# Performance work log

Measured on AMD Instinct MI355X. Metric: run time of the kernel, lower is better.

Reference implementation:

```python
import jax, jax.numpy as jnp
import numpy as np

NUM_HEADS = 8
B, S, D = 4, 2048, 512


def setup_inputs() -> dict:
    key = jax.random.key(0)
    ks = jax.random.split(key, 12)
    scale = 1.0 / np.sqrt(D)
    return {
        "v": jax.random.normal(ks[0], (B, S, D), dtype=jnp.float32),
        "k": jax.random.normal(ks[1], (B, S, D), dtype=jnp.float32),
        "q": jax.random.normal(ks[2], (B, S, D), dtype=jnp.float32),
        "Wq": jax.random.normal(ks[3], (D, D), dtype=jnp.float32) * scale,
        "bq": jnp.zeros((D,), dtype=jnp.float32),
        "Wk": jax.random.normal(ks[4], (D, D), dtype=jnp.float32) * scale,
        "bk": jnp.zeros((D,), dtype=jnp.float32),
        "Wv": jax.random.normal(ks[5], (D, D), dtype=jnp.float32) * scale,
        "bv": jnp.zeros((D,), dtype=jnp.float32),
        "Wo": jax.random.normal(ks[6], (D, D), dtype=jnp.float32) * scale,
        "bo": jnp.zeros((D,), dtype=jnp.float32),
        "top_k": 32,
    }


def reference(v, k, q, Wq, bq, Wk, bk, Wv, bv, Wo, bo, top_k):
    dh = D // NUM_HEADS  # per-head depth

    def split_heads(x):  # [B,S,D] -> [B,H,S,dh]
        return x.reshape(B, -1, NUM_HEADS, dh).transpose(0, 2, 1, 3)

    qh = split_heads(q @ Wq + bq)
    kh = split_heads(k @ Wk + bk)
    vh = split_heads(v @ Wv + bv)

    logits = jnp.einsum('bhqd,bhkd->bhqk', qh, kh) / jnp.sqrt(jnp.float32(dh))
    w = jax.nn.softmax(logits, axis=-1)  # [B,H,S,S]

    num_keys = w.shape[-1]
    if top_k < num_keys:
        vals, idx = jax.lax.top_k(w, top_k)  # [B,H,S,top_k]
        bb = jnp.arange(B)[:, None, None, None]
        hh = jnp.arange(NUM_HEADS)[None, :, None, None]
        qq = jnp.arange(S)[None, None, :, None]
        sparse = jnp.zeros_like(w).at[bb, hh, qq, idx].set(vals)
        # tf.linalg.normalize(ord=1): divide by L1 norm along last axis
        w = sparse / jnp.sum(jnp.abs(sparse), axis=-1, keepdims=True)

    attn = jnp.einsum('bhqk,bhkd->bhqd', w, vh)  # [B,H,S,dh]
    concat = attn.transpose(0, 2, 1, 3).reshape(B, -1, D)
    out = concat @ Wo + bo
    return (out, w)
```

## Files before the change

kernel.cpp:

```cpp
#include <hip/hip_runtime.h>
#include <hip/hip_bf16.h>
#include <stdint.h>

#define S_LEN 2048
#define DMODEL 512
#define NH 8
#define DH 64
#define TOPK 32
#define CMAX 128
#define LO_SCALE 4096.0f
#define INV_LO (1.0f/4096.0f)

typedef _Float16 f16;
typedef f16 half8 __attribute__((ext_vector_type(8)));
typedef f16 half4 __attribute__((ext_vector_type(4)));
typedef float floatx4 __attribute__((ext_vector_type(4)));
typedef float f32x4 __attribute__((ext_vector_type(4)));

#define AS1 __attribute__((address_space(1)))
#define AS3 __attribute__((address_space(3)))

__device__ __forceinline__ void gl_lds16(const void* g, void* l) {
    __builtin_amdgcn_global_load_lds((const AS1 void*)g, (AS3 void*)l, 16, 0, 0);
}
__device__ __forceinline__ void lds_fence() {
    asm volatile("s_waitcnt lgkmcnt(0)" ::: "memory");
}

__global__ __launch_bounds__(256, 2)
void qkproj(const float* __restrict__ Xq, const float* __restrict__ Xk,
            const float* __restrict__ Wq_, const float* __restrict__ Wk_,
            const float* __restrict__ bq_, const float* __restrict__ bk_,
            float* __restrict__ outQ, float* __restrict__ outK)
{
    __shared__ float As[32][132];
    __shared__ float Bs[32][264];
    const float* X    = blockIdx.z ? Xk  : Xq;
    const float* W    = blockIdx.z ? Wk_ : Wq_;
    const float* bias = blockIdx.z ? bk_ : bq_;
    float* out        = blockIdx.z ? outK : outQ;
    const int tid = threadIdx.x;
    const int tx = tid & 15;
    const int ty = tid >> 4;
    const int m0 = blockIdx.y * 128;
    const int n0 = blockIdx.x * 256;

    float acc[8][16];
#pragma unroll
    for (int i = 0; i < 8; ++i)
#pragma unroll
        for (int j = 0; j < 16; ++j) acc[i][j] = 0.f;

    f32x4 pa[4];
#pragma unroll
    for (int u = 0; u < 4; ++u) {
        int id = tid + u * 256;
        pa[u] = *(const f32x4*)(X + (size_t)(m0 + (id >> 3)) * 512 + (id & 7) * 4);
    }

    for (int k0 = 0; k0 < 512; k0 += 32) {
#pragma unroll
        for (int u = 0; u < 4; ++u) {
            int id = tid + u * 256;
            int r = id >> 3, c4 = (id & 7) * 4;
            As[c4 + 0][r] = pa[u].x; As[c4 + 1][r] = pa[u].y;
            As[c4 + 2][r] = pa[u].z; As[c4 + 3][r] = pa[u].w;
        }
#pragma unroll
        for (int u = 0; u < 8; ++u) {
            int id = tid + u * 256;
            int rb = id >> 6, cb = (id & 63) * 4;
            *(f32x4*)&Bs[rb][cb] = *(const f32x4*)(W + (size_t)(k0 + rb) * 512 + n0 + cb);
        }
        __syncthreads();
        if (k0 < 480) {
            int kn = k0 + 32;
#pragma unroll
            for (int u = 0; u < 4; ++u) {
                int id = tid + u * 256;
                pa[u] = *(const f32x4*)(X + (size_t)(m0 + (id >> 3)) * 512 + kn + (id & 7) * 4);
            }
        }
#pragma unroll 8
        for (int kk = 0; kk < 32; ++kk) {
            float a[8], b[16];
            *(f32x4*)&a[0] = *(const f32x4*)&As[kk][ty * 4];
            *(f32x4*)&a[4] = *(const f32x4*)&As[kk][64 + ty * 4];
#pragma unroll
            for (int h = 0; h < 4; ++h)
                *(f32x4*)&b[h * 4] = *(const f32x4*)&Bs[kk][tx * 4 + h * 64];
#pragma unroll
            for (int i = 0; i < 8; ++i)
#pragma unroll
                for (int j = 0; j < 16; ++j)
                    acc[i][j] = fmaf(a[i], b[j], acc[i][j]);
        }
        __syncthreads();
    }

    float bb[16];
#pragma unroll
    for (int h = 0; h < 4; ++h)
        *(f32x4*)&bb[h * 4] = *(const f32x4*)(bias + n0 + h * 64 + tx * 4);

#pragma unroll
    for (int i = 0; i < 8; ++i) {
        int r = m0 + (i >> 2) * 64 + ty * 4 + (i & 3);
        int b_ = r >> 11, s = r & 2047;
#pragma unroll
        for (int h = 0; h < 4; ++h) {
            int c = n0 + h * 64 + tx * 4;
            f32x4 w = {acc[i][h * 4 + 0] + bb[h * 4 + 0],
                       acc[i][h * 4 + 1] + bb[h * 4 + 1],
                       acc[i][h * 4 + 2] + bb[h * 4 + 2],
                       acc[i][h * 4 + 3] + bb[h * 4 + 3]};
            int hd = c >> 6, d = c & 63;
            float* p = out + (((size_t)(b_ * NH + hd) * S_LEN) + s) * DH + d;
            *(f32x4*)p = w;
        }
    }
}

__global__ __launch_bounds__(256, 2)
void gemm_logits(const float* __restrict__ Qh, const float* __restrict__ Kh,
                 float* __restrict__ logits)
{
    __shared__ float As[32][132];
    __shared__ float Bs[32][260];
    const int tid = threadIdx.x;
    const int tx = tid & 15;
    const int ty = tid >> 4;
    const int bh = blockIdx.z;
    const float* Ab = Qh + (size_t)bh * S_LEN * DH;
    const float* Bb = Kh + (size_t)bh * S_LEN * DH;
    const int q0 = blockIdx.y * 128;
    const int k0 = blockIdx.x * 256;

    float acc[8][16];
#pragma unroll
    for (int i = 0; i < 8; ++i)
#pragma unroll
        for (int j = 0; j < 16; ++j) acc[i][j] = 0.f;

    f32x4 qa[4], kb[8];
#pragma unroll
    for (int u = 0; u < 4; ++u) {
        int id = tid + u * 256;
        qa[u] = *(const f32x4*)(Ab + (size_t)(q0 + (id >> 3)) * DH + (id & 7) * 4);
    }
#pragma unroll
    for (int u = 0; u < 8; ++u) {
        int id = tid + u * 256;
        kb[u] = *(const f32x4*)(Bb + (size_t)(k0 + (id >> 3)) * DH + (id & 7) * 4);
    }

    for (int ch = 0; ch < 2; ++ch) {
#pragma unroll
        for (int u = 0; u < 4; ++u) {
            int id = tid + u * 256;
            int r = id >> 3, c4 = (id & 7) * 4;
            As[c4 + 0][r] = qa[u].x * 0.125f; As[c4 + 1][r] = qa[u].y * 0.125f;
            As[c4 + 2][r] = qa[u].z * 0.125f; As[c4 + 3][r] = qa[u].w * 0.125f;
        }
#pragma unroll
        for (int u = 0; u < 8; ++u) {
            int id = tid + u * 256;
            int r = id >> 3, c4 = (id & 7) * 4;
            Bs[c4 + 0][r] = kb[u].x; Bs[c4 + 1][r] = kb[u].y;
            Bs[c4 + 2][r] = kb[u].z; Bs[c4 + 3][r] = kb[u].w;
        }
        __syncthreads();
        if (ch == 0) {
#pragma unroll
            for (int u = 0; u < 4; ++u) {
                int id = tid + u * 256;
                qa[u] = *(const f32x4*)(Ab + (size_t)(q0 + (id >> 3)) * DH + 32 + (id & 7) * 4);
            }
#pragma unroll
            for (int u = 0; u < 8; ++u) {
                int id = tid + u * 256;
                kb[u] = *(const f32x4*)(Bb + (size_t)(k0 + (id >> 3)) * DH + 32 + (id & 7) * 4);
            }
        }
#pragma unroll 8
        for (int kk = 0; kk < 32; ++kk) {
            float a[8], b[16];
            *(f32x4*)&a[0] = *(const f32x4*)&As[kk][ty * 4];
            *(f32x4*)&a[4] = *(const f32x4*)&As[kk][64 + ty * 4];
#pragma unroll
            for (int h = 0; h < 4; ++h)
                *(f32x4*)&b[h * 4] = *(const f32x4*)&Bs[kk][tx * 4 + h * 64];
#pragma unroll
            for (int i = 0; i < 8; ++i)
#pragma unroll
                for (int j = 0; j < 16; ++j)
                    acc[i][j] = fmaf(a[i], b[j], acc[i][j]);
        }
        __syncthreads();
    }

#pragma unroll
    for (int i = 0; i < 8; ++i) {
        int r = q0 + (i >> 2) * 64 + ty * 4 + (i & 3);
        float* C = logits + (size_t)bh * S_LEN * S_LEN + (size_t)r * S_LEN + k0;
#pragma unroll
        for (int h = 0; h < 4; ++h) {
            f32x4 v = {acc[i][h * 4 + 0], acc[i][h * 4 + 1],
                       acc[i][h * 4 + 2], acc[i][h * 4 + 3]};
            __builtin_nontemporal_store(v, (f32x4*)(C + h * 64 + tx * 4));
        }
    }
}

__global__ __launch_bounds__(256)
void wsplit2(const float* __restrict__ W0, const float* __restrict__ W1,
             f16* __restrict__ planes)
{
    __shared__ float tile[32][33];
    const float* W = blockIdx.z ? W1 : W0;
    f16* Th = planes + (size_t)blockIdx.z * 524288;
    f16* Tl = Th + 262144;
    const int bx = blockIdx.x * 32;
    const int by = blockIdx.y * 32;
    const int lx = threadIdx.x & 31, ly = threadIdx.x >> 5;
#pragma unroll
    for (int r = ly; r < 32; r += 8)
        tile[r][lx] = W[(size_t)(by + r) * 512 + bx + lx];
    __syncthreads();
#pragma unroll
    for (int r = ly; r < 32; r += 8) {
        float x = tile[lx][r];
        f16 h = (f16)x;
        f16 l = (f16)((x - (float)h) * LO_SCALE);
        Th[(size_t)(bx + r) * 512 + by + lx] = h;
        Tl[(size_t)(bx + r) * 512 + by + lx] = l;
    }
}

__global__ __launch_bounds__(256)
void gemm_x32(const float* __restrict__ X,
              const f16* __restrict__ Bh_, const f16* __restrict__ Bl_,
              const float* __restrict__ bias, float* __restrict__ outF, int mode)
{
    __shared__ f16 sm[16384];
    f16* As_h = sm;       f16* As_l = sm + 4096;
    f16* Bs_h = sm + 8192; f16* Bs_l = sm + 12288;
    const int tid  = threadIdx.x;
    const int lane = tid & 63, wv = tid >> 6;
    const int wm = wv & 1, wn = wv >> 1;
    const int quad = lane >> 4, l15 = lane & 15;
    const int m0 = blockIdx.y * 128, n0 = blockIdx.x * 128;

    floatx4 acc_h[4][4], acc_c[4][4];
    const floatx4 z4 = {0.f, 0.f, 0.f, 0.f};
#pragma unroll
    for (int i = 0; i < 4; ++i)
#pragma unroll
        for (int j = 0; j < 4; ++j) { acc_h[i][j] = z4; acc_c[i][j] = z4; }

    for (int k0 = 0; k0 < 512; k0 += 32) {
        __syncthreads();
#pragma unroll
        for (int c = 0; c < 4; ++c) {
            int r   = c * 32 + (tid >> 3);
            int col = (tid & 7) * 4;
            f32x4 x = *(const f32x4*)(X + (size_t)(m0 + r) * 512 + k0 + col);
            f16 h0 = (f16)x.x, h1 = (f16)x.y, h2 = (f16)x.z, h3 = (f16)x.w;
            half4 hv = {h0, h1, h2, h3};
            half4 lv = {(f16)((x.x - (float)h0) * LO_SCALE),
                        (f16)((x.y - (float)h1) * LO_SCALE),
                        (f16)((x.z - (float)h2) * LO_SCALE),
                        (f16)((x.w - (float)h3) * LO_SCALE)};
            *(half4*)&As_h[r * 32 + col] = hv;
            *(half4*)&As_l[r * 32 + col] = lv;
        }
#pragma unroll
        for (int c = 0; c < 2; ++c) {
            int r    = c * 64 + (wv << 4) + (lane >> 2);
            int ch   = (lane & 3) * 8;
            int lidx = (c * 64 + (wv << 4)) * 32 + lane * 8;
            gl_lds16(Bh_ + (size_t)(n0 + r) * 512 + k0 + ch, &Bs_h[lidx]);
            gl_lds16(Bl_ + (size_t)(n0 + r) * 512 + k0 + ch, &Bs_l[lidx]);
        }
        asm volatile("s_waitcnt vmcnt(0)" ::: "memory");
        __syncthreads();

        half8 bh8[4], bl8[4];
#pragma unroll
        for (int j = 0; j < 4; ++j) {
            int n = wn * 64 + j * 16 + l15;
            bh8[j] = *(const half8*)&Bs_h[n * 32 + quad * 8];
            bl8[j] = *(const half8*)&Bs_l[n * 32 + quad * 8];
        }
#pragma unroll
        for (int i = 0; i < 4; ++i) {
            int m = wm * 64 + i * 16 + l15;
            half8 ah = *(const half8*)&As_h[m * 32 + quad * 8];
            half8 al = *(const half8*)&As_l[m * 32 + quad * 8];
#pragma unroll
            for (int j = 0; j < 4; ++j) {
                acc_h[i][j] = __builtin_amdgcn_mfma_f32_16x16x32_f16(ah, bh8[j], acc_h[i][j], 0, 0, 0);
                acc_c[i][j] = __builtin_amdgcn_mfma_f32_16x16x32_f16(ah, bl8[j], acc_c[i][j], 0, 0, 0);
                acc_c[i][j] = __builtin_amdgcn_mfma_f32_16x16x32_f16(al, bh8[j], acc_c[i][j], 0, 0, 0);
            }
        }
    }

#pragma unroll
    for (int j = 0; j < 4; ++j) {
        int col = n0 + wn * 64 + j * 16 + l15;
        float bv = bias[col];
#pragma unroll
        for (int i = 0; i < 4; ++i) {
            int rbase = m0 + wm * 64 + i * 16 + quad * 4;
#pragma unroll
            for (int rg = 0; rg < 4; ++rg) {
                float r = acc_h[i][j][rg] + acc_c[i][j][rg] * INV_LO + bv;
                int row = rbase + rg;
                if (mode == 2) {
                    outF[(size_t)row * 512 + col] = r;
                } else {
                    int b_ = row >> 11, s = row & 2047, h = col >> 6, d = col & 63;
                    outF[(((size_t)(b_ * NH + h)) * S_LEN + s) * DH + d] = r;
                }
            }
        }
    }
}

__global__ __launch_bounds__(256)
void gemm_x16(const f16* __restrict__ Ah_, const f16* __restrict__ Al_,
              const f16* __restrict__ Bh_, const f16* __restrict__ Bl_,
              const float* __restrict__ bias, float* __restrict__ outF,
              int Ksz, int ldc, int mode)
{
    __shared__ f16 sm[16384];
    f16* As_h = sm;        f16* As_l = sm + 4096;
    f16* Bs_h = sm + 8192; f16* Bs_l = sm + 12288;
    const int tid  = threadIdx.x;
    const int lane = tid & 63, wv = tid >> 6;
    const int wm = wv & 1, wn = wv >> 1;
    const int quad = lane >> 4, l15 = lane & 15;
    const int m0 = blockIdx.y * 128, n0 = blockIdx.x * 128;

    floatx4 acc_h[4][4], acc_c[4][4];
    const floatx4 z4 = {0.f, 0.f, 0.f, 0.f};
#pragma unroll
    for (int i = 0; i < 4; ++i)
#pragma unroll
        for (int j = 0; j < 4; ++j) { acc_h[i][j] = z4; acc_c[i][j] = z4; }

    for (int k0 = 0; k0 < Ksz; k0 += 32) {
        __syncthreads();
#pragma unroll
        for (int c = 0; c < 2; ++c) {
            int r    = c * 64 + (wv << 4) + (lane >> 2);
            int ch   = (lane & 3) * 8;
            int lidx = (c * 64 + (wv << 4)) * 32 + lane * 8;
            gl_lds16(Ah_ + (size_t)(m0 + r) * Ksz + k0 + ch, &As_h[lidx]);
            gl_lds16(Al_ + (size_t)(m0 + r) * Ksz + k0 + ch, &As_l[lidx]);
            gl_lds16(Bh_ + (size_t)(n0 + r) * Ksz + k0 + ch, &Bs_h[lidx]);
            gl_lds16(Bl_ + (size_t)(n0 + r) * Ksz + k0 + ch, &Bs_l[lidx]);
        }
        asm volatile("s_waitcnt vmcnt(0)" ::: "memory");
        __syncthreads();

        half8 bh8[4], bl8[4];
#pragma unroll
        for (int j = 0; j < 4; ++j) {
            int n = wn * 64 + j * 16 + l15;
            bh8[j] = *(const half8*)&Bs_h[n * 32 + quad * 8];
            bl8[j] = *(const half8*)&Bs_l[n * 32 + quad * 8];
        }
#pragma unroll
        for (int i = 0; i < 4; ++i) {
            int m = wm * 64 + i * 16 + l15;
            half8 ah = *(const half8*)&As_h[m * 32 + quad * 8];
            half8 al = *(const half8*)&As_l[m * 32 + quad * 8];
#pragma unroll
            for (int j = 0; j < 4; ++j) {
                acc_h[i][j] = __builtin_amdgcn_mfma_f32_16x16x32_f16(ah, bh8[j], acc_h[i][j], 0, 0, 0);
                acc_c[i][j] = __builtin_amdgcn_mfma_f32_16x16x32_f16(ah, bl8[j], acc_c[i][j], 0, 0, 0);
                acc_c[i][j] = __builtin_amdgcn_mfma_f32_16x16x32_f16(al, bh8[j], acc_c[i][j], 0, 0, 0);
            }
        }
    }

#pragma unroll
    for (int j = 0; j < 4; ++j) {
        int col = n0 + wn * 64 + j * 16 + l15;
        float bv = (mode == 2) ? bias[col] : 0.f;
#pragma unroll
        for (int i = 0; i < 4; ++i) {
            int rbase = m0 + wm * 64 + i * 16 + quad * 4;
#pragma unroll
            for (int rg = 0; rg < 4; ++rg) {
                float r = acc_h[i][j][rg] + acc_c[i][j][rg] * INV_LO;
                int row = rbase + rg;
                outF[(size_t)row * ldc + col] = r + bv;
            }
        }
    }
}

__device__ __forceinline__ unsigned sortable_u(float f) {
    unsigned u = __float_as_uint(f);
    return u ^ ((unsigned)(((int)u) >> 31) | 0x80000000u);
}

__global__ __launch_bounds__(256)
void topk_attn(float* __restrict__ wbuf, const float* __restrict__ Vh,
               f16* __restrict__ attH, f16* __restrict__ attL)
{
    __shared__ float    wrow[4][2048];
    __shared__ uint64_t cand[4][CMAX];
    __shared__ float    win_w[4][TOPK];
    __shared__ int      win_i[4][TOPK];

    const int tid  = threadIdx.x;
    const int wv   = tid >> 6;
    const int lane = tid & 63;
    const unsigned long long lt = (1ull << lane) - 1ull;
    const int row = blockIdx.x * 4 + wv;
    float* wr = wbuf + (size_t)row * 2048;

    if (lane < TOPK) { win_w[wv][lane] = 0.f; win_i[wv][lane] = 0; }

    float L[32];
#pragma unroll
    for (int t = 0; t < 8; ++t) {
        f32x4 x = __builtin_nontemporal_load((const f32x4*)(wr + t * 256 + lane * 4));
        L[4 * t + 0] = x.x; L[4 * t + 1] = x.y; L[4 * t + 2] = x.z; L[4 * t + 3] = x.w;
    }

    const f32x4 z = {0.f, 0.f, 0.f, 0.f};
#pragma unroll
    for (int t = 0; t < 8; ++t) ((f32x4*)wrow[wv])[t * 64 + lane] = z;

    float m = L[0];
#pragma unroll
    for (int t = 1; t < 32; ++t) m = fmaxf(m, L[t]);
#pragma unroll
    for (int off = 32; off > 0; off >>= 1) m = fmaxf(m, __shfl_xor(m, off, 64));

    auto wcount = [&](float T) -> int {
        int c = 0;
#pragma unroll
        for (int t = 0; t < 32; ++t) c += (int)__popcll(__ballot(L[t] >= T));
        return c;
    };

    float delta = 2.f;
    int clo = wcount(m - delta);
    int guard = 0;
    while (clo < TOPK && guard < 8) { delta *= 16.f; clo = wcount(m - delta); ++guard; }
    float Tlo = m - delta, Thi = m;
    guard = 0;
    while (clo > 64 && guard < 40) {
        float mid = 0.5f * (Tlo + Thi);
        int cc = wcount(mid);
        if (cc >= TOPK) { Tlo = mid; clo = cc; } else { Thi = mid; }
        ++guard;
    }
    const int nc = min(clo, CMAX);

    int base = 0;
#pragma unroll
    for (int t = 0; t < 32; ++t) {
        bool p = (L[t] >= Tlo);
        unsigned long long mk = __ballot(p);
        if (p) {
            int pos = base + (int)__popcll(mk & lt);
            if (pos < CMAX) {
                int idx = (t >> 2) * 256 + (lane << 2) + (t & 3);
                cand[wv][pos] = ((uint64_t)sortable_u(L[t]) << 32) | (uint32_t)(~(uint32_t)idx);
            }
        }
        base += (int)__popcll(mk);
    }
    lds_fence();

    float mysum = 0.f;
    int wbase = 0;
    const int passes = (nc + 63) >> 6;
    for (int it = 0; it < passes; ++it) {
        int ci = (it << 6) + lane;
        bool have = ci < nc;
        uint64_t mykey = have ? cand[wv][ci] : 0ull;
        int rank = 0;
#pragma unroll 8
        for (int j = 0; j < nc; ++j)
            rank += (cand[wv][j] > mykey) ? 1 : 0;
        bool win = have && (rank < TOPK);
        unsigned long long mk = __ballot(win);
        if (win) {
            int pos = wbase + (int)__popcll(mk & lt);
            unsigned uv = (unsigned)(mykey >> 32);
            unsigned fu = (uv & 0x80000000u) ? (uv ^ 0x80000000u) : ~uv;
            float v = __uint_as_float(fu);
            int idx = (int)(~(uint32_t)mykey);
            float e = __expf(v - m);
            win_w[wv][pos] = e;
            win_i[wv][pos] = idx;
            mysum += e;
        }
        wbase += (int)__popcll(mk);
    }
#pragma unroll
    for (int off = 32; off > 0; off >>= 1) mysum += __shfl_xor(mysum, off, 64);
    const float rw = 1.f / mysum;
    lds_fence();

    if (lane < TOPK) wrow[wv][win_i[wv][lane] & 2047] = win_w[wv][lane] * rw;
    lds_fence();

#pragma unroll
    for (int t = 0; t < 8; ++t)
        __builtin_nontemporal_store(((f32x4*)wrow[wv])[t * 64 + lane],
                                    (f32x4*)(wr + (size_t)(t * 64 + lane) * 4));

    const int bh = row >> 11;
    const float* Vb = Vh + (size_t)bh * S_LEN * DH;
    float acc = 0.f;
#pragma unroll
    for (int j = 0; j < TOPK; ++j) {
        float wj = win_w[wv][j] * rw;
        int   kj = win_i[wv][j];
        acc = fmaf(wj, Vb[(size_t)kj * DH + lane], acc);
    }
    const int b_ = row >> 14;
    const int h  = (row >> 11) & 7;
    const int s  = row & 2047;
    size_t oidx = (((size_t)b_ * S_LEN) + s) * 512 + h * DH + lane;
    f16 hh = (f16)acc;
    attH[oidx] = hh;
    attL[oidx] = (f16)((acc - (float)hh) * LO_SCALE);
}

extern "C" void kernel_launch(void* const* d_in, const int* in_sizes, int n_in,
                              void* d_out, int out_size, void* d_ws, size_t ws_size,
                              hipStream_t stream) {
    const float* v  = (const float*)d_in[0];
    const float* k  = (const float*)d_in[1];
    const float* q  = (const float*)d_in[2];
    const float* Wq = (const float*)d_in[3];
    const float* bq = (const float*)d_in[4];
    const float* Wk = (const float*)d_in[5];
    const float* bk = (const float*)d_in[6];
    const float* Wv = (const float*)d_in[7];
    const float* bv = (const float*)d_in[8];
    const float* Wo = (const float*)d_in[9];
    const float* bo = (const float*)d_in[10];

    float* out  = (float*)d_out;
    float* wout = out + (size_t)4 * S_LEN * 512;

    char* ws = (char*)d_ws;
    float* Vh   = (float*)ws;
    float* Qh32 = (float*)(ws + 16777216);
    float* Kh32 = (float*)(ws + 33554432);
    f16* WT  = (f16*)(ws + 50331648);
    f16 *WvH = WT,           *WvL = WT + 262144;
    f16 *WoH = WT + 524288,  *WoL = WT + 786432;
    f16* attH = (f16*)(ws + 16777216);
    f16* attL = (f16*)(ws + 25165824);

    wsplit2<<<dim3(16, 16, 2), 256, 0, stream>>>(Wv, Wo, WT);

    qkproj<<<dim3(2, 64, 2), 256, 0, stream>>>(q, k, Wq, Wk, bq, bk, Qh32, Kh32);
    gemm_x32<<<dim3(4, 64), 256, 0, stream>>>(v, WvH, WvL, bv, Vh, 1);

    gemm_logits<<<dim3(8, 16, 32), 256, 0, stream>>>(Qh32, Kh32, wout);

    topk_attn<<<16384, 256, 0, stream>>>(wout, Vh, attH, attL);

    gemm_x16<<<dim3(4, 64, 1), 256, 0, stream>>>(attH, attL, WoH, WoL, bo, out, 512, 512, 2);
}
```

Baseline: 1.120 ms.

## Fuse top-k selection into logits GEMM and shrink qkproj tile

The logits kernel now loops over all 2048 keys per 128-query block and keeps a running per-row top-32 list using a register bitonic sort plus a ballot-based insertion. This avoids writing and re-reading the full 2048x2048 logits matrix per head. Only the 32 packed key/index pairs are written to the start of each row, and a slimmer scatter kernel turns them into softmax weights and the dense output row. qkproj also drops to a 128-wide N tile with register-prefetched W loads. In exchange the grid is much smaller (512 blocks) and the serial insertion loop can diverge, so occupancy and latency hiding may suffer.

```diff
diff --git a/kernel.cpp b/kernel.cpp
--- a/kernel.cpp
+++ b/kernel.cpp
@@ -7,7 +7,6 @@
 #define NH 8
 #define DH 64
 #define TOPK 32
-#define CMAX 128
 #define LO_SCALE 4096.0f
 #define INV_LO (1.0f/4096.0f)
 
@@ -16,6 +15,7 @@
 typedef f16 half4 __attribute__((ext_vector_type(4)));
 typedef float floatx4 __attribute__((ext_vector_type(4)));
 typedef float f32x4 __attribute__((ext_vector_type(4)));
+typedef unsigned long long u64k;
 
 #define AS1 __attribute__((address_space(1)))
 #define AS3 __attribute__((address_space(3)))
@@ -27,14 +27,20 @@
     asm volatile("s_waitcnt lgkmcnt(0)" ::: "memory");
 }
 
-__global__ __launch_bounds__(256, 2)
+__device__ __forceinline__ u64k make_key(float f, int idx) {
+    unsigned u = __float_as_uint(f);
+    unsigned sv = u ^ ((unsigned)(((int)u) >> 31) | 0x80000000u);
+    return ((u64k)sv << 16) | (u64k)(0xFFFFu - (unsigned)idx);
+}
+
+__global__ __launch_bounds__(256)
 void qkproj(const float* __restrict__ Xq, const float* __restrict__ Xk,
             const float* __restrict__ Wq_, const float* __restrict__ Wk_,
             const float* __restrict__ bq_, const float* __restrict__ bk_,
             float* __restrict__ outQ, float* __restrict__ outK)
 {
     __shared__ float As[32][132];
-    __shared__ float Bs[32][264];
+    __shared__ float Bs[32][132];
     const float* X    = blockIdx.z ? Xk  : Xq;
     const float* W    = blockIdx.z ? Wk_ : Wq_;
     const float* bias = blockIdx.z ? bk_ : bq_;
@@ -43,19 +49,20 @@
     const int tx = tid & 15;
     const int ty = tid >> 4;
     const int m0 = blockIdx.y * 128;
-    const int n0 = blockIdx.x * 256;
-
-    float acc[8][16];
+    const int n0 = blockIdx.x * 128;
+
+    float acc[8][8];
 #pragma unroll
     for (int i = 0; i < 8; ++i)
 #pragma unroll
-        for (int j = 0; j < 16; ++j) acc[i][j] = 0.f;
-
-    f32x4 pa[4];
+        for (int j = 0; j < 8; ++j) acc[i][j] = 0.f;
+
+    f32x4 pa[4], pb[4];
 #pragma unroll
     for (int u = 0; u < 4; ++u) {
         int id = tid + u * 256;
         pa[u] = *(const f32x4*)(X + (size_t)(m0 + (id >> 3)) * 512 + (id & 7) * 4);
+        pb[u] = *(const f32x4*)(W + (size_t)(id >> 5) * 512 + n0 + (id & 31) * 4);
     }
 
     for (int k0 = 0; k0 < 512; k0 += 32) {
@@ -65,12 +72,8 @@
             int r = id >> 3, c4 = (id & 7) * 4;
             As[c4 + 0][r] = pa[u].x; As[c4 + 1][r] = pa[u].y;
             As[c4 + 2][r] = pa[u].z; As[c4 + 3][r] = pa[u].w;
-        }
-#pragma unroll
-        for (int u = 0; u < 8; ++u) {
-            int id = tid + u * 256;
-            int rb = id >> 6, cb = (id & 63) * 4;
-            *(f32x4*)&Bs[rb][cb] = *(const f32x4*)(W + (size_t)(k0 + rb) * 512 + n0 + cb);
+            int rb = id >> 5, cb = (id & 31) * 4;
+            *(f32x4*)&Bs[rb][cb] = pb[u];
         }
         __syncthreads();
         if (k0 < 480) {
@@ -79,36 +82,35 @@
             for (int u = 0; u < 4; ++u) {
                 int id = tid + u * 256;
                 pa[u] = *(const f32x4*)(X + (size_t)(m0 + (id >> 3)) * 512 + kn + (id & 7) * 4);
+                pb[u] = *(const f32x4*)(W + (size_t)(kn + (id >> 5)) * 512 + n0 + (id & 31) * 4);
             }
         }
 #pragma unroll 8
         for (int kk = 0; kk < 32; ++kk) {
-            float a[8], b[16];
+            float a[8], b[8];
             *(f32x4*)&a[0] = *(const f32x4*)&As[kk][ty * 4];
             *(f32x4*)&a[4] = *(const f32x4*)&As[kk][64 + ty * 4];
-#pragma unroll
-            for (int h = 0; h < 4; ++h)
-                *(f32x4*)&b[h * 4] = *(const f32x4*)&Bs[kk][tx * 4 + h * 64];
+            *(f32x4*)&b[0] = *(const f32x4*)&Bs[kk][tx * 4];
+            *(f32x4*)&b[4] = *(const f32x4*)&Bs[kk][64 + tx * 4];
 #pragma unroll
             for (int i = 0; i < 8; ++i)
 #pragma unroll
-                for (int j = 0; j < 16; ++j)
+                for (int j = 0; j < 8; ++j)
                     acc[i][j] = fmaf(a[i], b[j], acc[i][j]);
         }
         __syncthreads();
     }
 
-    float bb[16];
-#pragma unroll
-    for (int h = 0; h < 4; ++h)
-        *(f32x4*)&bb[h * 4] = *(const f32x4*)(bias + n0 + h * 64 + tx * 4);
+    float bb[8];
+    *(f32x4*)&bb[0] = *(const f32x4*)(bias + n0 + tx * 4);
+    *(f32x4*)&bb[4] = *(const f32x4*)(bias + n0 + 64 + tx * 4);
 
 #pragma unroll
     for (int i = 0; i < 8; ++i) {
-        int r = m0 + (i >> 2) * 64 + ty * 4 + (i & 3);
+        int r = m0 + ((i >> 2) << 6) + ty * 4 + (i & 3);
         int b_ = r >> 11, s = r & 2047;
 #pragma unroll
-        for (int h = 0; h < 4; ++h) {
+        for (int h = 0; h < 2; ++h) {
             int c = n0 + h * 64 + tx * 4;
             f32x4 w = {acc[i][h * 4 + 0] + bb[h * 4 + 0],
                        acc[i][h * 4 + 1] + bb[h * 4 + 1],
@@ -122,19 +124,19 @@
 }
 
 __global__ __launch_bounds__(256, 2)
-void gemm_logits(const float* __restrict__ Qh, const float* __restrict__ Kh,
-                 float* __restrict__ logits)
+void logits_topk(const float* __restrict__ Qh, const float* __restrict__ Kh,
+                 float* __restrict__ wbuf)
 {
-    __shared__ float As[32][132];
+    __shared__ float As[2][32][132];
     __shared__ float Bs[32][260];
     const int tid = threadIdx.x;
-    const int tx = tid & 15;
-    const int ty = tid >> 4;
-    const int bh = blockIdx.z;
+    const int lig = tid & 15;
+    const int ty  = tid >> 4;
+    const int gsh = ((tid & 63) >> 4) << 4;
+    const int bh = blockIdx.y;
+    const int q0 = blockIdx.x * 128;
     const float* Ab = Qh + (size_t)bh * S_LEN * DH;
     const float* Bb = Kh + (size_t)bh * S_LEN * DH;
-    const int q0 = blockIdx.y * 128;
-    const int k0 = blockIdx.x * 256;
 
     float acc[8][16];
 #pragma unroll
@@ -142,73 +144,144 @@
 #pragma unroll
         for (int j = 0; j < 16; ++j) acc[i][j] = 0.f;
 
-    f32x4 qa[4], kb[8];
-#pragma unroll
-    for (int u = 0; u < 4; ++u) {
-        int id = tid + u * 256;
-        qa[u] = *(const f32x4*)(Ab + (size_t)(q0 + (id >> 3)) * DH + (id & 7) * 4);
-    }
-#pragma unroll
-    for (int u = 0; u < 8; ++u) {
-        int id = tid + u * 256;
-        kb[u] = *(const f32x4*)(Bb + (size_t)(k0 + (id >> 3)) * DH + (id & 7) * 4);
-    }
-
-    for (int ch = 0; ch < 2; ++ch) {
-#pragma unroll
-        for (int u = 0; u < 4; ++u) {
-            int id = tid + u * 256;
-            int r = id >> 3, c4 = (id & 7) * 4;
-            As[c4 + 0][r] = qa[u].x * 0.125f; As[c4 + 1][r] = qa[u].y * 0.125f;
-            As[c4 + 2][r] = qa[u].z * 0.125f; As[c4 + 3][r] = qa[u].w * 0.125f;
-        }
+    u64k key0[8], key1[8];
+#pragma unroll
+    for (int i = 0; i < 8; ++i) { key0[i] = 0; key1[i] = 0; }
+
+    {
+        const int c4 = lig * 4;
+        const int ch = c4 >> 5;
+        const int cl = c4 & 31;
 #pragma unroll
         for (int u = 0; u < 8; ++u) {
-            int id = tid + u * 256;
-            int r = id >> 3, c4 = (id & 7) * 4;
-            Bs[c4 + 0][r] = kb[u].x; Bs[c4 + 1][r] = kb[u].y;
-            Bs[c4 + 2][r] = kb[u].z; Bs[c4 + 3][r] = kb[u].w;
-        }
-        __syncthreads();
-        if (ch == 0) {
-#pragma unroll
-            for (int u = 0; u < 4; ++u) {
-                int id = tid + u * 256;
-                qa[u] = *(const f32x4*)(Ab + (size_t)(q0 + (id >> 3)) * DH + 32 + (id & 7) * 4);
-            }
+            int r = ty + u * 16;
+            f32x4 x = *(const f32x4*)(Ab + (size_t)(q0 + r) * DH + c4);
+            As[ch][cl + 0][r] = x.x * 0.125f;
+            As[ch][cl + 1][r] = x.y * 0.125f;
+            As[ch][cl + 2][r] = x.z * 0.125f;
+            As[ch][cl + 3][r] = x.w * 0.125f;
+        }
+    }
+
+#pragma unroll 1
+    for (int kp = 0; kp < 8; ++kp) {
+#pragma unroll
+        for (int ch = 0; ch < 2; ++ch) {
+            f32x4 kb[8];
 #pragma unroll
             for (int u = 0; u < 8; ++u) {
                 int id = tid + u * 256;
-                kb[u] = *(const f32x4*)(Bb + (size_t)(k0 + (id >> 3)) * DH + 32 + (id & 7) * 4);
-            }
-        }
+                int r = id >> 3, c4 = (id & 7) * 4;
+                kb[u] = *(const f32x4*)(Bb + (size_t)(kp * 256 + r) * DH + ch * 32 + c4);
+            }
+            __syncthreads();
+#pragma unroll
+            for (int u = 0; u < 8; ++u) {
+                int id = tid + u * 256;
+                int r = id >> 3, c4 = (id & 7) * 4;
+                Bs[c4 + 0][r] = kb[u].x; Bs[c4 + 1][r] = kb[u].y;
+                Bs[c4 + 2][r] = kb[u].z; Bs[c4 + 3][r] = kb[u].w;
+            }
+            __syncthreads();
 #pragma unroll 8
-        for (int kk = 0; kk < 32; ++kk) {
-            float a[8], b[16];
-            *(f32x4*)&a[0] = *(const f32x4*)&As[kk][ty * 4];
-            *(f32x4*)&a[4] = *(const f32x4*)&As[kk][64 + ty * 4];
-#pragma unroll
-            for (int h = 0; h < 4; ++h)
-                *(f32x4*)&b[h * 4] = *(const f32x4*)&Bs[kk][tx * 4 + h * 64];
-#pragma unroll
-            for (int i = 0; i < 8; ++i)
-#pragma unroll
-                for (int j = 0; j < 16; ++j)
-                    acc[i][j] = fmaf(a[i], b[j], acc[i][j]);
-        }
-        __syncthreads();
+            for (int kk = 0; kk < 32; ++kk) {
+                float a[8], b[16];
+                *(f32x4*)&a[0] = *(const f32x4*)&As[ch][kk][ty * 4];
+                *(f32x4*)&a[4] = *(const f32x4*)&As[ch][kk][64 + ty * 4];
+#pragma unroll
+                for (int h = 0; h < 4; ++h)
+                    *(f32x4*)&b[h * 4] = *(const f32x4*)&Bs[kk][lig * 4 + h * 64];
+#pragma unroll
+                for (int i = 0; i < 8; ++i)
+#pragma unroll
+                    for (int j = 0; j < 16; ++j)
+                        acc[i][j] = fmaf(a[i], b[j], acc[i][j]);
+            }
+        }
+
+#pragma unroll
+        for (int i = 0; i < 8; ++i) {
+            int j0 = -1, j1 = -1;
+            if (kp == 0) {
+                u64k t0 = 0, t1 = 0;
+#pragma unroll
+                for (int j = 0; j < 16; ++j) {
+                    u64k kj = make_key(acc[i][j], ((j >> 2) << 6) + (lig << 2) + (j & 3));
+                    if (kj > t0)      { t1 = t0; j1 = j0; t0 = kj; j0 = j; }
+                    else if (kj > t1) { t1 = kj; j1 = j; }
+                }
+                key0[i] = t0; key1[i] = t1;
+#pragma unroll
+                for (int s = 2; s <= 32; s <<= 1) {
+#pragma unroll
+                    for (int d = s >> 1; d >= 1; d >>= 1) {
+                        int e0 = 2 * lig;
+                        if (d == 1) {
+                            bool descB = ((e0 & s) == 0);
+                            u64k mx = key0[i] > key1[i] ? key0[i] : key1[i];
+                            u64k mn = key0[i] > key1[i] ? key1[i] : key0[i];
+                            key0[i] = descB ? mx : mn;
+                            key1[i] = descB ? mn : mx;
+                        } else {
+                            bool descB = ((e0 & s) == 0);
+                            bool amS   = ((e0 & d) == 0);
+                            bool wantMax = (descB == amS);
+                            u64k p0 = __shfl_xor(key0[i], d >> 1, 16);
+                            u64k p1 = __shfl_xor(key1[i], d >> 1, 16);
+                            key0[i] = wantMax ? (key0[i] > p0 ? key0[i] : p0)
+                                              : (key0[i] > p0 ? p0 : key0[i]);
+                            key1[i] = wantMax ? (key1[i] > p1 ? key1[i] : p1)
+                                              : (key1[i] > p1 ? p1 : key1[i]);
+                        }
+                    }
+                }
+            }
+            u64k bot0 = __shfl(key1[i], 15, 16);
+            unsigned pend = 0;
+#pragma unroll
+            for (int j = 0; j < 16; ++j) {
+                u64k kj = make_key(acc[i][j], kp * 256 + ((j >> 2) << 6) + (lig << 2) + (j & 3));
+                if (kj > bot0 && j != j0 && j != j1) pend |= (1u << j);
+            }
+            for (int it = 0; it < 300; ++it) {
+                unsigned long long wb = __ballot(pend != 0);
+                unsigned gm = (unsigned)((wb >> gsh) & 0xFFFFull);
+                if (!gm) break;
+                int src = __ffs((int)gm) - 1;
+                int myj = __ffs((int)pend) - 1;
+                float mv = acc[i][0];
+#pragma unroll
+                for (int j = 1; j < 16; ++j) if (myj == j) mv = acc[i][j];
+                int jj = myj < 0 ? 0 : myj;
+                u64k ck = make_key(mv, kp * 256 + ((jj >> 2) << 6) + (lig << 2) + (jj & 3));
+                ck = __shfl(ck, src, 16);
+                if (lig == src) pend &= pend - 1;
+                u64k bt = __shfl(key1[i], 15, 16);
+                if (ck <= bt) continue;
+                unsigned long long b0 = __ballot(key0[i] > ck);
+                unsigned long long b1 = __ballot(key1[i] > ck);
+                int pos = __popcll((b0 >> gsh) & 0xFFFFull)
+                        + __popcll((b1 >> gsh) & 0xFFFFull);
+                u64k up = __shfl_up(key1[i], 1, 16);
+                int e0 = 2 * lig, e1 = e0 + 1;
+                u64k nk0 = (e0 < pos) ? key0[i] : ((e0 == pos) ? ck : up);
+                u64k nk1 = (e1 < pos) ? key1[i] : ((e1 == pos) ? ck : key0[i]);
+                key0[i] = nk0; key1[i] = nk1;
+            }
+        }
+
+#pragma unroll
+        for (int i = 0; i < 8; ++i)
+#pragma unroll
+            for (int j = 0; j < 16; ++j) acc[i][j] = 0.f;
     }
 
 #pragma unroll
     for (int i = 0; i < 8; ++i) {
-        int r = q0 + (i >> 2) * 64 + ty * 4 + (i & 3);
-        float* C = logits + (size_t)bh * S_LEN * S_LEN + (size_t)r * S_LEN + k0;
-#pragma unroll
-        for (int h = 0; h < 4; ++h) {
-            f32x4 v = {acc[i][h * 4 + 0], acc[i][h * 4 + 1],
-                       acc[i][h * 4 + 2], acc[i][h * 4 + 3]};
-            __builtin_nontemporal_store(v, (f32x4*)(C + h * 64 + tx * 4));
-        }
+        int r = q0 + ((i >> 2) << 6) + ty * 4 + (i & 3);
+        float* wr = wbuf + ((size_t)bh * S_LEN + r) * S_LEN;
+        *(u64k*)(wr + (lig << 2))     = key0[i];
+        *(u64k*)(wr + (lig << 2) + 2) = key1[i];
     }
 }
 
@@ -403,115 +476,42 @@
     }
 }
 
-__device__ __forceinline__ unsigned sortable_u(float f) {
-    unsigned u = __float_as_uint(f);
-    return u ^ ((unsigned)(((int)u) >> 31) | 0x80000000u);
-}
-
 __global__ __launch_bounds__(256)
-void topk_attn(float* __restrict__ wbuf, const float* __restrict__ Vh,
-               f16* __restrict__ attH, f16* __restrict__ attL)
+void topk_scatter(float* __restrict__ wbuf, const float* __restrict__ Vh,
+                  f16* __restrict__ attH, f16* __restrict__ attL)
 {
-    __shared__ float    wrow[4][2048];
-    __shared__ uint64_t cand[4][CMAX];
-    __shared__ float    win_w[4][TOPK];
-    __shared__ int      win_i[4][TOPK];
+    __shared__ float wrow[4][2048];
+    __shared__ float win_w[4][TOPK];
+    __shared__ int   win_i[4][TOPK];
 
     const int tid  = threadIdx.x;
     const int wv   = tid >> 6;
     const int lane = tid & 63;
-    const unsigned long long lt = (1ull << lane) - 1ull;
-    const int row = blockIdx.x * 4 + wv;
+    const int row  = blockIdx.x * 4 + wv;
     float* wr = wbuf + (size_t)row * 2048;
 
-    if (lane < TOPK) { win_w[wv][lane] = 0.f; win_i[wv][lane] = 0; }
-
-    float L[32];
-#pragma unroll
-    for (int t = 0; t < 8; ++t) {
-        f32x4 x = __builtin_nontemporal_load((const f32x4*)(wr + t * 256 + lane * 4));
-        L[4 * t + 0] = x.x; L[4 * t + 1] = x.y; L[4 * t + 2] = x.z; L[4 * t + 3] = x.w;
-    }
-
-    const f32x4 z = {0.f, 0.f, 0.f, 0.f};
-#pragma unroll
-    for (int t = 0; t < 8; ++t) ((f32x4*)wrow[wv])[t * 64 + lane] = z;
-
-    float m = L[0];
-#pragma unroll
-    for (int t = 1; t < 32; ++t) m = fmaxf(m, L[t]);
-#pragma unroll
-    for (int off = 32; off > 0; off >>= 1) m = fmaxf(m, __shfl_xor(m, off, 64));
-
-    auto wcount = [&](float T) -> int {
-        int c = 0;
-#pragma unroll
-        for (int t = 0; t < 32; ++t) c += (int)__popcll(__ballot(L[t] >= T));
-        return c;
-    };
-
-    float delta = 2.f;
-    int clo = wcount(m - delta);
-    int guard = 0;
-    while (clo < TOPK && guard < 8) { delta *= 16.f; clo = wcount(m - delta); ++guard; }
-    float Tlo = m - delta, Thi = m;
-    guard = 0;
-    while (clo > 64 && guard < 40) {
-        float mid = 0.5f * (Tlo + Thi);
-        int cc = wcount(mid);
-        if (cc >= TOPK) { Tlo = mid; clo = cc; } else { Thi = mid; }
-        ++guard;
-    }
-    const int nc = min(clo, CMAX);
-
-    int base = 0;
-#pragma unroll
-    for (int t = 0; t < 32; ++t) {
-        bool p = (L[t] >= Tlo);
-        unsigned long long mk = __ballot(p);
-        if (p) {
-            int pos = base + (int)__popcll(mk & lt);
-            if (pos < CMAX) {
-                int idx = (t >> 2) * 256 + (lane << 2) + (t & 3);
-                cand[wv][pos] = ((uint64_t)sortable_u(L[t]) << 32) | (uint32_t)(~(uint32_t)idx);
-            }
-        }
-        base += (int)__popcll(mk);
-    }
-    lds_fence();
-
-    float mysum = 0.f;
-    int wbase = 0;
-    const int passes = (nc + 63) >> 6;
-    for (int it = 0; it < passes; ++it) {
-        int ci = (it << 6) + lane;
-        bool have = ci < nc;
-        uint64_t mykey = have ? cand[wv][ci] : 0ull;
-        int rank = 0;
-#pragma unroll 8
-        for (int j = 0; j < nc; ++j)
-            rank += (cand[wv][j] > mykey) ? 1 : 0;
-        bool win = have && (rank < TOPK);
-        unsigned long long mk = __ballot(win);
-        if (win) {
-            int pos = wbase + (int)__popcll(mk & lt);
-            unsigned uv = (unsigned)(mykey >> 32);
-            unsigned fu = (uv & 0x80000000u) ? (uv ^ 0x80000000u) : ~uv;
-            float v = __uint_as_float(fu);
-            int idx = (int)(~(uint32_t)mykey);
-            float e = __expf(v - m);
-            win_w[wv][pos] = e;
-            win_i[wv][pos] = idx;
-            mysum += e;
-        }
-        wbase += (int)__popcll(mk);
-    }
+    u64k key = 0;
+    if (lane < TOPK) key = ((const u64k*)wr)[lane];
+    unsigned sv = (unsigned)(key >> 16);
+    unsigned fu = (sv & 0x80000000u) ? (sv ^ 0x80000000u) : ~sv;
+    float v = __uint_as_float(fu);
+    int idx = (int)(0xFFFFu - (unsigned)(key & 0xFFFFull)) & 2047;
+
+    float m = __shfl(v, 0, 64);
+    float e = (lane < TOPK) ? __expf(v - m) : 0.f;
+
+    float mysum = e;
 #pragma unroll
     for (int off = 32; off > 0; off >>= 1) mysum += __shfl_xor(mysum, off, 64);
     const float rw = 1.f / mysum;
+
+    if (lane < TOPK) { win_w[wv][lane] = e; win_i[wv][lane] = idx; }
+
+    const f32x4 z = {0.f, 0.f, 0.f, 0.f};
+#pragma unroll
+    for (int t = 0; t < 8; ++t) ((f32x4*)wrow[wv])[t * 64 + lane] = z;
     lds_fence();
-
-    if (lane < TOPK) wrow[wv][win_i[wv][lane] & 2047] = win_w[wv][lane] * rw;
+    if (lane < TOPK) wrow[wv][win_i[wv][lane]] = win_w[wv][lane] * rw;
     lds_fence();
 
 #pragma unroll
@@ -567,12 +567,12 @@
 
     wsplit2<<<dim3(16, 16, 2), 256, 0, stream>>>(Wv, Wo, WT);
 
-    qkproj<<<dim3(2, 64, 2), 256, 0, stream>>>(q, k, Wq, Wk, bq, bk, Qh32, Kh32);
+    qkproj<<<dim3(4, 64, 2), 256, 0, stream>>>(q, k, Wq, Wk, bq, bk, Qh32, Kh32);
     gemm_x32<<<dim3(4, 64), 256, 0, stream>>>(v, WvH, WvL, bv, Vh, 1);
 
-    gemm_logits<<<dim3(8, 16, 32), 256, 0, stream>>>(Qh32, Kh32, wout);
-
-    topk_attn<<<16384, 256, 0, stream>>>(wout, Vh, attH, attL);
+    logits_topk<<<dim3(16, 32), 256, 0, stream>>>(Qh32, Kh32, wout);
+
+    topk_scatter<<<16384, 256, 0, stream>>>(wout, Vh, attH, attL);
 
     gemm_x16<<<dim3(4, 64, 1), 256, 0, stream>>>(attH, attL, WoH, WoL, bo, out, 512, 512, 2);
 }
```

After: 1.779 ms. 58.8% more time.
